# Performance work log

Measured on AMD Instinct MI355X. Metric: run time of the kernel, lower is better.

Reference implementation:

```python
import jax, jax.numpy as jnp
import numpy as np
import math

DIM = 256; SEQ = 2048; BSZ = 32; NI = 128; NS = 4; ITERS = 3

def _ln(x, g, b):
    m = x.mean(-1, keepdims=True)
    v = ((x - m) ** 2).mean(-1, keepdims=True)
    return (x - m) / jnp.sqrt(v + 1e-5) * g + b

def _norm(x):
    # torch F.normalize: x / ||x||.clamp_min(1e-12)
    return x / jnp.clip(jnp.linalg.norm(x, axis=-1, keepdims=True), 1e-12, None)

def setup_inputs() -> dict:
    key = jax.random.key(0)
    ks = jax.random.split(key, 16)
    def w(k, shape, s=0.02):
        return jax.random.normal(k, shape, jnp.float32) * s
    return {
        'tokens': jax.random.normal(ks[0], (BSZ, SEQ, DIM), jnp.float32),
        'cls_embed': jax.random.normal(ks[1], (BSZ, DIM), jnp.float32),
        'intent_queries': jax.random.normal(ks[2], (NI, DIM), jnp.float32),
        'noise': jax.random.normal(ks[3], (NI, BSZ, NS, DIM), jnp.float32),
        'Wk': w(ks[4], (DIM, DIM)), 'bk': jnp.zeros(DIM, jnp.float32),
        'Wv': w(ks[5], (DIM, DIM)), 'bv': jnp.zeros(DIM, jnp.float32),
        'Wqs': w(ks[6], (DIM, DIM)), 'bqs': jnp.zeros(DIM, jnp.float32),
        'Wqi': w(ks[7], (DIM, DIM)), 'bqi': jnp.zeros(DIM, jnp.float32),
        'ln1_g': jnp.ones(DIM, jnp.float32), 'ln1_b': jnp.zeros(DIM, jnp.float32),
        'ln2_g': jnp.ones(DIM, jnp.float32), 'ln2_b': jnp.zeros(DIM, jnp.float32),
        'Wf1': w(ks[8], (DIM, 2 * DIM)), 'bf1': jnp.zeros(2 * DIM, jnp.float32),
        'Wf2': w(ks[9], (2 * DIM, DIM)), 'bf2': jnp.zeros(DIM, jnp.float32),
        'slot_mu': w(ks[10], (1, NS, DIM)),  # randn*0.02
        'slot_sigma': jnp.ones((1, NS, DIM), jnp.float32) * 0.1,
        'alpha': jnp.float32(1.0),
        'temperature': jnp.float32(1.0),
    }

def reference(tokens, cls_embed, intent_queries, noise, Wk, bk, Wv, bv,
              Wqs, bqs, Wqi, bqi, ln1_g, ln1_b, ln2_g, ln2_b,
              Wf1, bf1, Wf2, bf2, slot_mu, slot_sigma, alpha, temperature):
    scale = 1.0 / math.sqrt(DIM)
    # k/v are identical across the per-intent loop in the original -> compute once
    k = tokens @ Wk + bk  # [B,S,D]
    v = tokens @ Wv + bv  # [B,S,D]
    cls_n = _norm(cls_embed)  # [B,D]

    def per_intent(q, eps):  # q: [D], eps: [B,NS,D]
        qn = _norm(q)
        q_intent = (q @ Wqi + bqi)[None, None, :]  # broadcast over [B,NS,:]
        slots = slot_mu[0] + eps * slot_sigma[0]   # [B,NS,D]
        for _ in range(ITERS):
            q_slot = slots @ Wqs + bqs + q_intent
            logit = jnp.einsum('bnd,bsd->bns', q_slot, k) * scale
            attn = jax.nn.softmax(logit, axis=-1)
            upd = jnp.einsum('bns,bsd->bnd', attn, v)
            slots = _ln(slots + upd, ln1_g, ln1_b)
            h = _ln(slots, ln2_g, ln2_b)
            slots = slots + jax.nn.gelu(h @ Wf1 + bf1, approximate=False) @ Wf2 + bf2
        sn = _norm(slots)                               # [B,NS,D]
        a = jax.nn.softmax(jnp.einsum('bnd,d->bn', sn, qn), axis=-1)
        summ = jnp.einsum('bn,bnd->bd', a, slots)       # slot_summary
        fused = cls_n + alpha * _norm(summ)
        return fused @ qn                               # [B]

    scores = jax.vmap(per_intent)(intent_queries, noise)  # [NI,B]
    logits = scores.T / jnp.maximum(temperature, 1e-4)    # [B,NI]
    return logits
```

## Files before the change

### kernel.cpp

```cpp
#include <hip/hip_runtime.h>
#include <math.h>

#define BSZ 32
#define NI  128

typedef __attribute__((ext_vector_type(8))) _Float16 f16x8;
typedef __attribute__((ext_vector_type(4))) _Float16 f16x4;
typedef __attribute__((ext_vector_type(4))) float    f32x4;

#define MFMA16(a, b, c) __builtin_amdgcn_mfma_f32_16x16x32_f16((a), (b), (c), 0, 0, 0)

#define GLL(g, l) __builtin_amdgcn_global_load_lds(                          \
    (const __attribute__((address_space(1))) void*)(g),                      \
    (__attribute__((address_space(3))) void*)(l), 16, 0, 0)

#define LGKM_BAR() do {                                                      \
    asm volatile("s_waitcnt lgkmcnt(0)" ::: "memory");                       \
    __builtin_amdgcn_sched_barrier(0);                                       \
    __builtin_amdgcn_s_barrier();                                            \
    __builtin_amdgcn_sched_barrier(0); } while (0)

__device__ inline float dot4f(float4 a, float4 b) {
    return a.x * b.x + a.y * b.y + a.z * b.z + a.w * b.w;
}

__device__ inline float4* slp(float* base, int r, int c) {
    return (float4*)(base + r * 256 + ((((c) >> 2) ^ (r & 7)) << 2));
}

__device__ inline void tpose64(const float* __restrict__ src, int Csrc,
                               _Float16* __restrict__ dstT, int KT,
                               int r0, int c0, _Float16 (*tbuf)[72], int tid)
{
#pragma unroll
    for (int it = 0; it < 4; it++) {
        int idx = tid + it * 256;
        int rr = idx >> 4, c4 = idx & 15;
        float4 w = *(const float4*)(src + (size_t)(r0 + rr) * Csrc + c0 + c4 * 4);
        tbuf[c4 * 4 + 0][rr] = (_Float16)w.x;
        tbuf[c4 * 4 + 1][rr] = (_Float16)w.y;
        tbuf[c4 * 4 + 2][rr] = (_Float16)w.z;
        tbuf[c4 * 4 + 3][rr] = (_Float16)w.w;
    }
    __syncthreads();
#pragma unroll
    for (int it = 0; it < 2; it++) {
        int idx = tid + it * 256;
        int orr = idx >> 3, oc8 = idx & 7;
        int n = c0 + orr;
        size_t tile = (size_t)(n >> 4) * KT + (r0 >> 5) + (oc8 >> 2);
        *(f16x8*)(dstT + tile * 512 + (n & 15) * 32 + (oc8 & 3) * 8) = *(const f16x8*)&tbuf[orr][oc8 * 8];
    }
}

__global__ __launch_bounds__(256) void prep(
    const float* __restrict__ Wk, const float* __restrict__ Wv,
    const float* __restrict__ Wqs, const float* __restrict__ Wf1,
    const float* __restrict__ Wf2,
    const float* __restrict__ intent_q, const float* __restrict__ Wqi,
    const float* __restrict__ bqi, const float* __restrict__ bqs,
    const float* __restrict__ cls_embed,
    _Float16* __restrict__ wkT, _Float16* __restrict__ wvT,
    _Float16* __restrict__ wqsT, _Float16* __restrict__ wf1T,
    _Float16* __restrict__ wf2T,
    float* __restrict__ qint2, float* __restrict__ qn, float* __restrict__ clsn)
{
    __shared__ _Float16 tbuf[64][72];
    __shared__ float buf[256];
    __shared__ float red[4];
    const int t = threadIdx.x, blk = blockIdx.x;
    const int lane = t & 63, w = t >> 6;

    if (blk < 112) {
        if (blk < 16)       tpose64(Wk, 256, wkT, 8, (blk >> 2) * 64, (blk & 3) * 64, tbuf, t);
        else if (blk < 32)  { int tt = blk - 16; tpose64(Wv, 256, wvT, 8, (tt >> 2) * 64, (tt & 3) * 64, tbuf, t); }
        else if (blk < 48)  { int tt = blk - 32; tpose64(Wqs, 256, wqsT, 8, (tt >> 2) * 64, (tt & 3) * 64, tbuf, t); }
        else if (blk < 80)  { int tt = blk - 48; tpose64(Wf1, 512, wf1T, 8, (tt & 3) * 64, (tt >> 2) * 64, tbuf, t); }
        else                { int tt = blk - 80; tpose64(Wf2, 256, wf2T, 16, (tt >> 2) * 64, (tt & 3) * 64, tbuf, t); }
    } else if (blk < 240) {
        int i = blk - 112;
        float x = intent_q[(size_t)i * 256 + t];
        buf[t] = x;
        float ss = x * x;
#pragma unroll
        for (int m = 1; m < 64; m <<= 1) ss += __shfl_xor(ss, m, 64);
        if (lane == 0) red[w] = ss;
        __syncthreads();
        float tot = red[0] + red[1] + red[2] + red[3];
        qn[(size_t)i * 256 + t] = x / fmaxf(sqrtf(tot), 1e-12f);
        float acc = bqi[t] + bqs[t];
        for (int e = 0; e < 256; e += 4) {
            const float4 q4 = *(const float4*)&buf[e];
            acc += q4.x * Wqi[(size_t)(e + 0) * 256 + t];
            acc += q4.y * Wqi[(size_t)(e + 1) * 256 + t];
            acc += q4.z * Wqi[(size_t)(e + 2) * 256 + t];
            acc += q4.w * Wqi[(size_t)(e + 3) * 256 + t];
        }
        qint2[(size_t)i * 256 + t] = acc;
    } else {
        int b = blk - 240;
        float x = cls_embed[(size_t)b * 256 + t];
        float ss = x * x;
#pragma unroll
        for (int m = 1; m < 64; m <<= 1) ss += __shfl_xor(ss, m, 64);
        if (lane == 0) red[w] = ss;
        __syncthreads();
        float tot = red[0] + red[1] + red[2] + red[3];
        clsn[(size_t)b * 256 + t] = x / fmaxf(sqrtf(tot), 1e-12f);
    }
}

__global__ __launch_bounds__(512, 2) void kvf_k(
    const float* __restrict__ tokens,
    const _Float16* __restrict__ wkT, const _Float16* __restrict__ wvT,
    const float* __restrict__ bk, const float* __restrict__ bv,
    _Float16* __restrict__ kT, _Float16* __restrict__ vT)
{
    __shared__ __align__(16) _Float16 Sb[2][8192];

    const int t = threadIdx.x, lane = t & 63, w = t >> 6;
    const int l15 = lane & 15, quad = lane >> 4;
    const int lofs = l15 * 32 + quad * 8;
    const int lofsA = ((l15 * 4 + quad) ^ ((l15 >> 1) & 7)) * 8;
    const int bx = blockIdx.x;
    const int b = bx & 31, chunk = bx >> 5;

    f16x8 wk[2][8], wv[2][8];
#pragma unroll
    for (int j = 0; j < 2; j++)
#pragma unroll
        for (int ks = 0; ks < 8; ks++) {
            wk[j][ks] = *(const f16x8*)(wkT + ((size_t)(2 * w + j) * 8 + ks) * 512 + lofs);
            wv[j][ks] = *(const f16x8*)(wvT + ((size_t)(2 * w + j) * 8 + ks) * 512 + lofs);
        }
    f32x4 bi0 = *(const f32x4*)(bk + w * 32 + quad * 4);
    f32x4 bi1 = *(const f32x4*)(bk + w * 32 + 16 + quad * 4);
    const float bv0 = bv[(2 * w) * 16 + l15];
    const float bv1 = bv[(2 * w + 1) * 16 + l15];

    const int rr = t >> 5, d8 = t & 31;
    const float* tbase = tokens + ((size_t)b * 2048 + chunk * 256) * 256 + rr * 256 + d8 * 8;
    const int mskW = ((rr >> 1) & 7) ^ (((d8 >> 2) & 3) << 1);
    const int wofs0 = (d8 >> 2) * 512 + (((rr * 4 + (d8 & 3)) ^ mskW) * 8);
    const int wofs1 = wofs0 + 8 * 512;

    float4 pa0, pa1, pb0, pb1;

#define KVF_LOADS(P) do {                                                    \
        const float* sp_ = tbase + (size_t)(P) * 8192;                       \
        pa0 = *(const float4*)(sp_);                                         \
        pa1 = *(const float4*)(sp_ + 4);                                     \
        pb0 = *(const float4*)(sp_ + 4096);                                  \
        pb1 = *(const float4*)(sp_ + 4100);                                  \
    } while (0)

#define KVF_STAGE(BUF) do {                                                  \
        f16x8 h0, h1;                                                        \
        h0[0] = (_Float16)pa0.x; h0[1] = (_Float16)pa0.y;                    \
        h0[2] = (_Float16)pa0.z; h0[3] = (_Float16)pa0.w;                    \
        h0[4] = (_Float16)pa1.x; h0[5] = (_Float16)pa1.y;                    \
        h0[6] = (_Float16)pa1.z; h0[7] = (_Float16)pa1.w;                    \
        h1[0] = (_Float16)pb0.x; h1[1] = (_Float16)pb0.y;                    \
        h1[2] = (_Float16)pb0.z; h1[3] = (_Float16)pb0.w;                    \
        h1[4] = (_Float16)pb1.x; h1[5] = (_Float16)pb1.y;                    \
        h1[6] = (_Float16)pb1.z; h1[7] = (_Float16)pb1.w;                    \
        *(f16x8*)((BUF) + wofs0) = h0;                                       \
        *(f16x8*)((BUF) + wofs1) = h1;                                       \
    } while (0)

    KVF_LOADS(0);
    KVF_STAGE(&Sb[0][0]);
    LGKM_BAR();

    for (int p = 0; p < 8; p++) {
        if (p < 7) KVF_LOADS(p + 1);
        __builtin_amdgcn_sched_barrier(0);

        const _Float16* lb = &Sb[p & 1][0];
        const int stg0 = chunk * 16 + p * 2;
        const int sp = chunk * 8 + p;

        f16x8 a[2][8];
#pragma unroll
        for (int st = 0; st < 2; st++)
#pragma unroll
            for (int ks = 0; ks < 8; ks++)
                a[st][ks] = *(const f16x8*)(lb + (st * 8 + ks) * 512 + (lofsA ^ ((ks & 3) * 16)));

#pragma unroll
        for (int st = 0; st < 2; st++) {
            f32x4 c0 = {0.f, 0.f, 0.f, 0.f}, c1 = {0.f, 0.f, 0.f, 0.f};
#pragma unroll
            for (int ks = 0; ks < 8; ks++) {
                c0 = MFMA16(wk[0][ks], a[st][ks], c0);
                c1 = MFMA16(wk[1][ks], a[st][ks], c1);
            }
            f16x4 p0, p1;
#pragma unroll
            for (int reg = 0; reg < 4; reg++) {
                p0[reg] = (_Float16)(c0[reg] + bi0[reg]);
                p1[reg] = (_Float16)(c1[reg] + bi1[reg]);
            }
            _Float16* tp = kT + ((size_t)(b * 128 + stg0 + st) * 8 + w) * 512 + l15 * 32;
            *(f16x4*)(tp + (quad >> 1) * 8 + (quad & 1) * 4) = p0;
            *(f16x4*)(tp + (2 + (quad >> 1)) * 8 + (quad & 1) * 4) = p1;
        }

#pragma unroll
        for (int j = 0; j < 2; j++) {
            f32x4 c0 = {0.f, 0.f, 0.f, 0.f}, c1 = {0.f, 0.f, 0.f, 0.f};
#pragma unroll
            for (int ks = 0; ks < 8; ks++) {
                c0 = MFMA16(a[0][ks], wv[j][ks], c0);
                c1 = MFMA16(a[1][ks], wv[j][ks], c1);
            }
            const float bb = j ? bv1 : bv0;
            f16x4 p0, p1;
#pragma unroll
            for (int reg = 0; reg < 4; reg++) {
                p0[reg] = (_Float16)(c0[reg] + bb);
                p1[reg] = (_Float16)(c1[reg] + bb);
            }
            _Float16* tp = vT + ((size_t)(b * 16 + 2 * w + j) * 64 + sp) * 512 + l15 * 32;
            *(f16x4*)(tp + (quad >> 1) * 8 + (quad & 1) * 4) = p0;
            *(f16x4*)(tp + (2 + (quad >> 1)) * 8 + (quad & 1) * 4) = p1;
        }

        if (p < 7) {
            KVF_STAGE(&Sb[(p + 1) & 1][0]);
            LGKM_BAR();
        }
    }
#undef KVF_LOADS
#undef KVF_STAGE
}

__global__ __launch_bounds__(256, 4) void slotq_k(
    const float* __restrict__ noise, const float* __restrict__ slot_mu,
    const float* __restrict__ slot_sigma,
    const _Float16* __restrict__ wqsT, const float* __restrict__ qint2,
    float* __restrict__ slots, _Float16* __restrict__ qsT)
{
    __shared__ float sb[16 * 256];
    const int tid = threadIdx.x, lane = tid & 63, w4 = tid >> 6;
    const int l15 = lane & 15, quad = lane >> 4;
    const int lofs = l15 * 32 + quad * 8;
    const int rt = blockIdx.x;
    const int gr0 = rt * 16;

    {
        const int lr = w4 * 4 + quad;
        const int gr = gr0 + lr;
        const int b = gr >> 9, i = (gr >> 2) & 127, n = gr & 3;
        const float* np = noise + (((size_t)i * BSZ + b) * 4 + n) * 256;
#pragma unroll
        for (int k = 0; k < 4; k++) {
            const int c = k * 64 + l15 * 4;
            float4 mu = *(const float4*)(slot_mu + n * 256 + c);
            float4 sg = *(const float4*)(slot_sigma + n * 256 + c);
            float4 ns = *(const float4*)(np + c);
            float4 o;
            o.x = mu.x + ns.x * sg.x; o.y = mu.y + ns.y * sg.y;
            o.z = mu.z + ns.z * sg.z; o.w = mu.w + ns.w * sg.w;
            *slp(sb, lr, c) = o;
            *(float4*)(slots + (size_t)gr * 256 + c) = o;
        }
    }
    __syncthreads();

    f16x8 bs[8];
#pragma unroll
    for (int ks = 0; ks < 8; ks++) {
        const int c0 = ks * 32 + quad * 8;
        float4 xa = *slp(sb, l15, c0);
        float4 xb = *slp(sb, l15, c0 + 4);
        bs[ks][0] = (_Float16)xa.x; bs[ks][1] = (_Float16)xa.y;
        bs[ks][2] = (_Float16)xa.z; bs[ks][3] = (_Float16)xa.w;
        bs[ks][4] = (_Float16)xb.x; bs[ks][5] = (_Float16)xb.y;
        bs[ks][6] = (_Float16)xb.z; bs[ks][7] = (_Float16)xb.w;
    }
    const int iq = ((gr0 + l15) & 511) >> 2;
#pragma unroll
    for (int d = 0; d < 4; d++) {
        const int dti = w4 * 4 + d;
        f32x4 c = {0.f, 0.f, 0.f, 0.f};
#pragma unroll
        for (int ks = 0; ks < 8; ks++)
            c = MFMA16(*(const f16x8*)(wqsT + ((size_t)dti * 8 + ks) * 512 + lofs), bs[ks], c);
        float4 qi = *(const float4*)(qint2 + (size_t)iq * 256 + dti * 16 + quad * 4);
        f16x4 o;
#pragma unroll
        for (int reg = 0; reg < 4; reg++) o[reg] = (_Float16)((c[reg] + qi[reg]) * 0.0625f);
        *(f16x4*)(qsT + ((size_t)rt * 8 + (dti >> 1)) * 512 + l15 * 32
                  + ((dti & 1) * 2 + (quad >> 1)) * 8 + (quad & 1) * 4) = o;
    }
}

__global__ __launch_bounds__(512, 2) void attn_k(
    const _Float16* __restrict__ qsT, const _Float16* __restrict__ kT,
    const _Float16* __restrict__ vT,
    _Float16* __restrict__ Opart, float* __restrict__ psum4)
{
    __shared__ __align__(16) _Float16 Kb[2][16384];
    __shared__ __align__(16) _Float16 Vb[16384];
    __shared__ __align__(16) _Float16 pb[8][2304];

    const int tid = threadIdx.x, lane = tid & 63, wv = tid >> 6;
    const int l15 = lane & 15, quad = lane >> 4;
    const int lofs = l15 * 32 + quad * 8;
    const int lofsA = ((l15 * 4 + quad) ^ ((l15 >> 1) & 7)) * 8;
    const int lnsw = (lane ^ ((lane >> 3) & 7)) * 8;
    const int bx = blockIdx.x;
    const int b = bx & 31, rb = (bx >> 5) & 1, sk = bx >> 6;
    const int gr0 = b * 512 + rb * 256 + wv * 32;
    const int rt_q = gr0 >> 4;

    _Float16* pw = pb[wv];

    const _Float16* kSrc = kT + ((size_t)(b * 128 + sk * 32) * 8) * 512;

    {
        const _Float16* src = kSrc + (size_t)(wv * 4) * 512 + lnsw;
        _Float16* dst = &Kb[0][(wv * 4) * 512 + lane * 8];
#pragma unroll
        for (int j = 0; j < 4; j++) GLL(src + j * 512, dst + j * 512);
    }

    f16x8 q[2][8];
#pragma unroll
    for (int m = 0; m < 2; m++)
#pragma unroll
        for (int ks = 0; ks < 8; ks++)
            q[m][ks] = *(const f16x8*)(qsT + ((size_t)(rt_q + m) * 8 + ks) * 512 + lofs);

    f32x4 O[2][16];
#pragma unroll
    for (int m = 0; m < 2; m++)
#pragma unroll
        for (int dt = 0; dt < 16; dt++) O[m][dt] = (f32x4){0.f, 0.f, 0.f, 0.f};
    float ps[2][4] = {{0.f, 0.f, 0.f, 0.f}, {0.f, 0.f, 0.f, 0.f}};

    asm volatile("s_waitcnt vmcnt(0)" ::: "memory");
    __builtin_amdgcn_s_barrier();
    __builtin_amdgcn_sched_barrier(0);

    for (int s = 0; s < 8; s++) {
        const int cur = s & 1;

        {
            const int seg0 = wv * 4;
#pragma unroll
            for (int j = 0; j < 4; j++) {
                const int seg = seg0 + j;
                const _Float16* src = vT
                    + ((size_t)(b * 16 + (seg >> 1)) * 64 + sk * 16 + s * 2 + (seg & 1)) * 512
                    + lnsw;
                GLL(src, &Vb[seg * 512 + lane * 8]);
            }
        }
        if (s < 7) {
            const _Float16* src = kSrc + (size_t)(s + 1) * 16384 + (wv * 4) * 512 + lnsw;
            _Float16* dst = &Kb[cur ^ 1][(wv * 4) * 512 + lane * 8];
#pragma unroll
            for (int j = 0; j < 4; j++) GLL(src + j * 512, dst + j * 512);
            asm volatile("s_waitcnt vmcnt(8)" ::: "memory");
        } else {
            asm volatile("s_waitcnt vmcnt(4)" ::: "memory");
        }
        __builtin_amdgcn_s_barrier();
        __builtin_amdgcn_sched_barrier(0);

#pragma unroll
        for (int kt = 0; kt < 4; kt++) {
            const _Float16* kp = &Kb[cur][(kt * 8) * 512];
            f32x4 c0 = {0.f, 0.f, 0.f, 0.f}, c1 = {0.f, 0.f, 0.f, 0.f};
#pragma unroll
            for (int ks = 0; ks < 8; ks++) {
                f16x8 kf = *(const f16x8*)(kp + ks * 512 + lofsA);
                c0 = MFMA16(q[0][ks], kf, c0);
                c1 = MFMA16(q[1][ks], kf, c1);
            }
            const int col = kt * 16 + l15;
#pragma unroll
            for (int reg = 0; reg < 4; reg++) {
                float p0 = __expf(fminf(c0[reg], 10.5f));
                float p1 = __expf(fminf(c1[reg], 10.5f));
                ps[0][reg] += p0;
                ps[1][reg] += p1;
                pw[(quad * 4 + reg) * 72 + col] = (_Float16)p0;
                pw[(16 + quad * 4 + reg) * 72 + col] = (_Float16)p1;
            }
        }

        __builtin_amdgcn_sched_barrier(0);
        if (s < 7) {
            asm volatile("s_waitcnt vmcnt(4)" ::: "memory");
        } else {
            asm volatile("s_waitcnt vmcnt(0)" ::: "memory");
        }
        __builtin_amdgcn_s_barrier();
        __builtin_amdgcn_sched_barrier(0);

        f16x8 pa[2][2];
#pragma unroll
        for (int m = 0; m < 2; m++)
#pragma unroll
            for (int kg = 0; kg < 2; kg++)
                pa[m][kg] = *(const f16x8*)(pw + (m * 16 + l15) * 72 + kg * 32 + quad * 8);
#pragma unroll
        for (int dt = 0; dt < 16; dt++) {
            const _Float16* vp = &Vb[dt * 1024];
            f16x8 v0 = *(const f16x8*)(vp + lofsA);
            f16x8 v1 = *(const f16x8*)(vp + 512 + lofsA);
            O[0][dt] = MFMA16(pa[0][0], v0, O[0][dt]);
            O[0][dt] = MFMA16(pa[0][1], v1, O[0][dt]);
            O[1][dt] = MFMA16(pa[1][0], v0, O[1][dt]);
            O[1][dt] = MFMA16(pa[1][1], v1, O[1][dt]);
        }

        __builtin_amdgcn_sched_barrier(0);
        __builtin_amdgcn_s_barrier();
        __builtin_amdgcn_sched_barrier(0);
    }

#pragma unroll
    for (int m = 0; m < 2; m++) {
#pragma unroll
        for (int msk = 1; msk <= 8; msk <<= 1)
#pragma unroll
            for (int reg = 0; reg < 4; reg++) ps[m][reg] += __shfl_xor(ps[m][reg], msk, 64);
        if (l15 == 0) {
#pragma unroll
            for (int reg = 0; reg < 4; reg++)
                psum4[(size_t)sk * 16384 + gr0 + m * 16 + quad * 4 + reg] = ps[m][reg];
        }
    }

#pragma unroll
    for (int m = 0; m < 2; m++) {
#pragma unroll
        for (int hd = 0; hd < 2; hd++) {
#pragma unroll
            for (int dt = 0; dt < 8; dt++) {
                const int dti = hd * 8 + dt;
#pragma unroll
                for (int reg = 0; reg < 4; reg++)
                    pw[(quad * 4 + reg) * 136 + dt * 16 + l15] = (_Float16)O[m][dti][reg];
            }
#pragma unroll
            for (int p2 = 0; p2 < 4; p2++) {
                const int u = lane + p2 * 64;
                const int row = u >> 4, col8 = u & 15;
                *(f16x8*)(Opart + ((size_t)sk * 16384 + gr0 + m * 16 + row) * 256 + hd * 128 + col8 * 8) =
                    *(const f16x8*)(pw + row * 136 + col8 * 8);
            }
        }
    }
}

__global__ __launch_bounds__(256, 4) void mlp_k(
    const _Float16* __restrict__ Opart, const float* __restrict__ psum4,
    float* __restrict__ slots,
    const float* __restrict__ ln1_g, const float* __restrict__ ln1_b,
    const float* __restrict__ ln2_g, const float* __restrict__ ln2_b,
    const _Float16* __restrict__ wf1T, const float* __restrict__ bf1,
    const _Float16* __restrict__ wf2T, const float* __restrict__ bf2,
    const _Float16* __restrict__ wqsT, const float* __restrict__ qint2,
    _Float16* __restrict__ qsT,
    const float* __restrict__ qn, const float* __restrict__ clsn,
    const float* __restrict__ alphap, const float* __restrict__ tempp,
    float* __restrict__ out, int it)
{
    __shared__ float sl[16 * 256];
    __shared__ float2 st2[16];
    __shared__ __align__(16) _Float16 actL[8192];

    const int tid = threadIdx.x, lane = tid & 63, w4 = tid >> 6;
    const int l15 = lane & 15, quad = lane >> 4;
    const int lofs = l15 * 32 + quad * 8;
    const int lofsA = ((l15 * 4 + quad) ^ ((l15 >> 1) & 7)) * 8;
    const int bx = blockIdx.x;
    const int b = bx & 31, rg = bx >> 5;
    const int R0 = b * 512 + rg * 16;

    {
        const int lr = w4 * 4 + quad;
        const int gr = R0 + lr;
        float l = 0.f;
#pragma unroll
        for (int j = 0; j < 4; j++) l += psum4[(size_t)j * 16384 + gr];
        const float invl = 1.f / l;
        float4 y[4];
        float sm = 0.f, sq = 0.f;
#pragma unroll
        for (int k = 0; k < 4; k++) {
            const int c = k * 64 + l15 * 4;
            float4 o4 = {0.f, 0.f, 0.f, 0.f};
#pragma unroll
            for (int j = 0; j < 4; j++) {
                f16x4 p = *(const f16x4*)(Opart + ((size_t)j * 16384 + gr) * 256 + c);
                o4.x += (float)p[0]; o4.y += (float)p[1];
                o4.z += (float)p[2]; o4.w += (float)p[3];
            }
            float4 s4 = *(const float4*)(slots + (size_t)gr * 256 + c);
            y[k].x = s4.x + o4.x * invl; y[k].y = s4.y + o4.y * invl;
            y[k].z = s4.z + o4.z * invl; y[k].w = s4.w + o4.w * invl;
            sm += y[k].x + y[k].y + y[k].z + y[k].w;
            sq += dot4f(y[k], y[k]);
        }
#pragma unroll
        for (int m = 1; m <= 8; m <<= 1) { sm += __shfl_xor(sm, m, 64); sq += __shfl_xor(sq, m, 64); }
        const float mean = sm * (1.f / 256.f);
        const float rstd = rsqrtf(sq * (1.f / 256.f) - mean * mean + 1e-5f);
        float sm2 = 0.f, sq2 = 0.f;
#pragma unroll
        for (int k = 0; k < 4; k++) {
            const int c = k * 64 + l15 * 4;
            float4 g1 = *(const float4*)(ln1_g + c);
            float4 b1 = *(const float4*)(ln1_b + c);
            float4 x1;
            x1.x = (y[k].x - mean) * rstd * g1.x + b1.x;
            x1.y = (y[k].y - mean) * rstd * g1.y + b1.y;
            x1.z = (y[k].z - mean) * rstd * g1.z + b1.z;
            x1.w = (y[k].w - mean) * rstd * g1.w + b1.w;
            *slp(sl, lr, c) = x1;
            sm2 += x1.x + x1.y + x1.z + x1.w;
            sq2 += dot4f(x1, x1);
        }
#pragma unroll
        for (int m = 1; m <= 8; m <<= 1) { sm2 += __shfl_xor(sm2, m, 64); sq2 += __shfl_xor(sq2, m, 64); }
        const float mean2 = sm2 * (1.f / 256.f);
        const float rstd2 = rsqrtf(sq2 * (1.f / 256.f) - mean2 * mean2 + 1e-5f);
        if (l15 == 0) st2[lr] = make_float2(mean2, rstd2);
    }
    __syncthreads();

    {
        const float2 s2 = st2[l15];
        f16x8 bh[8];
#pragma unroll
        for (int ks = 0; ks < 8; ks++) {
            const int c0 = ks * 32 + quad * 8;
            float4 xa = *slp(sl, l15, c0);
            float4 xb = *slp(sl, l15, c0 + 4);
            float4 ga = *(const float4*)(ln2_g + c0);
            float4 gb = *(const float4*)(ln2_g + c0 + 4);
            float4 ba = *(const float4*)(ln2_b + c0);
            float4 bb2 = *(const float4*)(ln2_b + c0 + 4);
            bh[ks][0] = (_Float16)((xa.x - s2.x) * s2.y * ga.x + ba.x);
            bh[ks][1] = (_Float16)((xa.y - s2.x) * s2.y * ga.y + ba.y);
            bh[ks][2] = (_Float16)((xa.z - s2.x) * s2.y * ga.z + ba.z);
            bh[ks][3] = (_Float16)((xa.w - s2.x) * s2.y * ga.w + ba.w);
            bh[ks][4] = (_Float16)((xb.x - s2.x) * s2.y * gb.x + bb2.x);
            bh[ks][5] = (_Float16)((xb.y - s2.x) * s2.y * gb.y + bb2.y);
            bh[ks][6] = (_Float16)((xb.z - s2.x) * s2.y * gb.z + bb2.z);
            bh[ks][7] = (_Float16)((xb.w - s2.x) * s2.y * gb.w + bb2.w);
        }
#pragma unroll 2
        for (int t8 = 0; t8 < 8; t8++) {
            const int hti = w4 * 8 + t8;
            f32x4 c = {0.f, 0.f, 0.f, 0.f};
#pragma unroll
            for (int ks = 0; ks < 8; ks++)
                c = MFMA16(*(const f16x8*)(wf1T + ((size_t)hti * 8 + ks) * 512 + lofs), bh[ks], c);
            float4 bb = *(const float4*)(bf1 + hti * 16 + quad * 4);
            f16x4 o;
#pragma unroll
            for (int reg = 0; reg < 4; reg++) {
                float xg = c[reg] + bb[reg];
                o[reg] = (_Float16)(0.5f * xg * (1.f + erff(xg * 0.70710678118654752f)));
            }
            const int gA = l15 * 4 + (hti & 1) * 2 + (quad >> 1);
            *(f16x4*)(actL + ((size_t)(hti >> 1)) * 512
                      + ((gA ^ ((l15 >> 1) & 7)) * 8) + (quad & 1) * 4) = o;
        }
    }
    __syncthreads();

    {
        f32x4 c[4];
#pragma unroll
        for (int d = 0; d < 4; d++) {
            const int dti = w4 * 4 + d;
            float4 x4 = *slp(sl, l15, dti * 16 + quad * 4);
            float4 bb = *(const float4*)(bf2 + dti * 16 + quad * 4);
            c[d] = (f32x4){x4.x + bb.x, x4.y + bb.y, x4.z + bb.z, x4.w + bb.w};
        }
        for (int ks = 0; ks < 16; ks++) {
            f16x8 afrag = *(const f16x8*)(actL + (size_t)ks * 512 + lofsA);
#pragma unroll
            for (int d = 0; d < 4; d++)
                c[d] = MFMA16(*(const f16x8*)(wf2T + ((size_t)(w4 * 4 + d) * 16 + ks) * 512 + lofs),
                              afrag, c[d]);
        }
        __syncthreads();
#pragma unroll
        for (int d = 0; d < 4; d++) {
            const int dti = w4 * 4 + d;
            float4 v = {c[d][0], c[d][1], c[d][2], c[d][3]};
            *slp(sl, l15, dti * 16 + quad * 4) = v;
        }
    }
    __syncthreads();

    if (it < 2) {
        f16x8 bs[8];
#pragma unroll
        for (int ks = 0; ks < 8; ks++) {
            const int c0 = ks * 32 + quad * 8;
            float4 xa = *slp(sl, l15, c0);
            float4 xb = *slp(sl, l15, c0 + 4);
            bs[ks][0] = (_Float16)xa.x; bs[ks][1] = (_Float16)xa.y;
            bs[ks][2] = (_Float16)xa.z; bs[ks][3] = (_Float16)xa.w;
            bs[ks][4] = (_Float16)xb.x; bs[ks][5] = (_Float16)xb.y;
            bs[ks][6] = (_Float16)xb.z; bs[ks][7] = (_Float16)xb.w;
        }
        const int iq = rg * 4 + (l15 >> 2);
        const int rtg = b * 32 + rg;
#pragma unroll
        for (int d = 0; d < 4; d++) {
            const int dti = w4 * 4 + d;
            f32x4 c = {0.f, 0.f, 0.f, 0.f};
#pragma unroll
            for (int ks = 0; ks < 8; ks++)
                c = MFMA16(*(const f16x8*)(wqsT + ((size_t)dti * 8 + ks) * 512 + lofs), bs[ks], c);
            float4 qi = *(const float4*)(qint2 + (size_t)iq * 256 + dti * 16 + quad * 4);
            f16x4 o;
#pragma unroll
            for (int reg = 0; reg < 4; reg++) o[reg] = (_Float16)((c[reg] + qi[reg]) * 0.0625f);
            *(f16x4*)(qsT + ((size_t)rtg * 8 + (dti >> 1)) * 512 + l15 * 32
                      + ((dti & 1) * 2 + (quad >> 1)) * 8 + (quad & 1) * 4) = o;
        }
        {
            const int lr2 = tid >> 4, c16 = tid & 15;
#pragma unroll
            for (int q4 = 0; q4 < 4; q4++) {
                float4 v = *slp(sl, lr2, c16 * 16 + q4 * 4);
                *(float4*)(slots + (size_t)(R0 + lr2) * 256 + c16 * 16 + q4 * 4) = v;
            }
        }
    } else {
        const int i = rg * 4 + w4;
        float4 qv = *(const float4*)(qn + (size_t)i * 256 + lane * 4);
        float4 xs[4];
        float st4[4];
#pragma unroll
        for (int n = 0; n < 4; n++) {
            xs[n] = *slp(sl, w4 * 4 + n, lane * 4);
            float ss = dot4f(xs[n], xs[n]);
            float sq = dot4f(xs[n], qv);
#pragma unroll
            for (int m = 1; m < 64; m <<= 1) { ss += __shfl_xor(ss, m, 64); sq += __shfl_xor(sq, m, 64); }
            st4[n] = sq / fmaxf(sqrtf(ss), 1e-12f);
        }
        float mx = fmaxf(fmaxf(st4[0], st4[1]), fmaxf(st4[2], st4[3]));
        float e0 = __expf(st4[0] - mx), e1 = __expf(st4[1] - mx);
        float e2 = __expf(st4[2] - mx), e3 = __expf(st4[3] - mx);
        float inv = 1.f / (e0 + e1 + e2 + e3);
        float4 smv;
        smv.x = (e0 * xs[0].x + e1 * xs[1].x + e2 * xs[2].x + e3 * xs[3].x) * inv;
        smv.y = (e0 * xs[0].y + e1 * xs[1].y + e2 * xs[2].y + e3 * xs[3].y) * inv;
        smv.z = (e0 * xs[0].z + e1 * xs[1].z + e2 * xs[2].z + e3 * xs[3].z) * inv;
        smv.w = (e0 * xs[0].w + e1 * xs[1].w + e2 * xs[2].w + e3 * xs[3].w) * inv;
        float ssm = dot4f(smv, smv);
        float sqn = dot4f(smv, qv);
        float4 cv = *(const float4*)(clsn + (size_t)b * 256 + lane * 4);
        float cq = dot4f(cv, qv);
#pragma unroll
        for (int m = 1; m < 64; m <<= 1) {
            ssm += __shfl_xor(ssm, m, 64);
            sqn += __shfl_xor(sqn, m, 64);
            cq  += __shfl_xor(cq,  m, 64);
        }
        if (lane == 0) {
            float score = cq + alphap[0] * sqn / fmaxf(sqrtf(ssm), 1e-12f);
            out[(size_t)b * NI + i] = score / fmaxf(tempp[0], 1e-4f);
        }
    }
}

extern "C" void kernel_launch(void* const* d_in, const int* in_sizes, int n_in,
                              void* d_out, int out_size, void* d_ws, size_t ws_size,
                              hipStream_t stream)
{
    const float* tokens     = (const float*)d_in[0];
    const float* cls_embed  = (const float*)d_in[1];
    const float* intent_q   = (const float*)d_in[2];
    const float* noise      = (const float*)d_in[3];
    const float* Wk  = (const float*)d_in[4];
    const float* bk  = (const float*)d_in[5];
    const float* Wv  = (const float*)d_in[6];
    const float* bv  = (const float*)d_in[7];
    const float* Wqs = (const float*)d_in[8];
    const float* bqs = (const float*)d_in[9];
    const float* Wqi = (const float*)d_in[10];
    const float* bqi = (const float*)d_in[11];
    const float* ln1g = (const float*)d_in[12];
    const float* ln1b = (const float*)d_in[13];
    const float* ln2g = (const float*)d_in[14];
    const float* ln2b = (const float*)d_in[15];
    const float* Wf1 = (const float*)d_in[16];
    const float* bf1 = (const float*)d_in[17];
    const float* Wf2 = (const float*)d_in[18];
    const float* bf2 = (const float*)d_in[19];
    const float* slot_mu    = (const float*)d_in[20];
    const float* slot_sigma = (const float*)d_in[21];
    const float* alphap = (const float*)d_in[22];
    const float* tempp  = (const float*)d_in[23];
    float* out = (float*)d_out;

    char* base = (char*)d_ws;
    _Float16* qsT   = (_Float16*)(base);
    _Float16* kT    = (_Float16*)(base + 33554432u);
    _Float16* vT    = (_Float16*)(base + 67108864u);
    _Float16* Opart = (_Float16*)(base + 100663296u);
    float* slots    = (float*)(base + 134217728u);
    _Float16* wkT   = (_Float16*)(base + 150994944u);
    _Float16* wvT   = (_Float16*)(base + 151126016u);
    _Float16* wqsT  = (_Float16*)(base + 151257088u);
    _Float16* wf1T  = (_Float16*)(base + 151388160u);
    _Float16* wf2T  = (_Float16*)(base + 151650304u);
    float* qint2    = (float*)(base + 151912448u);
    float* qnb      = (float*)(base + 152043520u);
    float* clsn     = (float*)(base + 152174592u);
    float* psum4    = (float*)(base + 152207360u);

    prep<<<272, 256, 0, stream>>>(Wk, Wv, Wqs, Wf1, Wf2, intent_q, Wqi, bqi, bqs,
                                  cls_embed, wkT, wvT, wqsT, wf1T, wf2T,
                                  qint2, qnb, clsn);
    kvf_k<<<256, 512, 0, stream>>>(tokens, wkT, wvT, bk, bv, kT, vT);
    slotq_k<<<1024, 256, 0, stream>>>(noise, slot_mu, slot_sigma, wqsT, qint2,
                                      slots, qsT);

    for (int it = 0; it < 3; it++) {
        attn_k<<<256, 512, 0, stream>>>(qsT, kT, vT, Opart, psum4);
        mlp_k<<<1024, 256, 0, stream>>>(Opart, psum4, slots,
                                        ln1g, ln1b, ln2g, ln2b,
                                        wf1T, bf1, wf2T, bf2,
                                        wqsT, qint2, qsT,
                                        qnb, clsn, alphap, tempp, out, it);
    }
}
```

Measured before the change: 473.6 us.

## Halve rows per wave in attention kernel to double grid and occupancy

The attention kernel now gives each wave 16 query rows instead of 32 and processes the key range in 16 smaller steps of 32 keys. It launches 512 blocks instead of 256 with launch bounds of 4 blocks per CU. Shared memory shrinks because the K, V and P buffers are smaller and the output staging reuses the K/V arena. The aim is higher occupancy and better latency hiding, at the cost of half the K/V reuse per block, twice as many global loads of K/V, and more barriers per key.

```diff
diff --git a/kernel.cpp b/kernel.cpp
--- a/kernel.cpp
+++ b/kernel.cpp
@@ -296,14 +296,16 @@
     }
 }
 
-__global__ __launch_bounds__(512, 2) void attn_k(
+__global__ __launch_bounds__(512, 4) void attn_k(
     const _Float16* __restrict__ qsT, const _Float16* __restrict__ kT,
     const _Float16* __restrict__ vT,
     _Float16* __restrict__ Opart, float* __restrict__ psum4)
 {
-    __shared__ __align__(16) _Float16 Kb[2][16384];
-    __shared__ __align__(16) _Float16 Vb[16384];
-    __shared__ __align__(16) _Float16 pb[8][2304];
+    __shared__ __align__(16) _Float16 arena[24576];
+    __shared__ __align__(16) _Float16 pb[8][640];
+
+    _Float16* KbA = arena;
+    _Float16* VbA = arena + 16384;
 
     const int tid = threadIdx.x, lane = tid & 63, wv = tid >> 6;
     const int l15 = lane & 15, quad = lane >> 4;
@@ -311,149 +313,121 @@
     const int lofsA = ((l15 * 4 + quad) ^ ((l15 >> 1) & 7)) * 8;
     const int lnsw = (lane ^ ((lane >> 3) & 7)) * 8;
     const int bx = blockIdx.x;
-    const int b = bx & 31, rb = (bx >> 5) & 1, sk = bx >> 6;
-    const int gr0 = b * 512 + rb * 256 + wv * 32;
+    const int b = bx & 31, rb = (bx >> 5) & 3, sk = bx >> 7;
+    const int gr0 = b * 512 + rb * 128 + wv * 16;
     const int rt_q = gr0 >> 4;
 
     _Float16* pw = pb[wv];
 
     const _Float16* kSrc = kT + ((size_t)(b * 128 + sk * 32) * 8) * 512;
-
-    {
-        const _Float16* src = kSrc + (size_t)(wv * 4) * 512 + lnsw;
-        _Float16* dst = &Kb[0][(wv * 4) * 512 + lane * 8];
-#pragma unroll
-        for (int j = 0; j < 4; j++) GLL(src + j * 512, dst + j * 512);
-    }
-
-    f16x8 q[2][8];
-#pragma unroll
-    for (int m = 0; m < 2; m++)
-#pragma unroll
-        for (int ks = 0; ks < 8; ks++)
-            q[m][ks] = *(const f16x8*)(qsT + ((size_t)(rt_q + m) * 8 + ks) * 512 + lofs);
-
-    f32x4 O[2][16];
-#pragma unroll
-    for (int m = 0; m < 2; m++)
-#pragma unroll
-        for (int dt = 0; dt < 16; dt++) O[m][dt] = (f32x4){0.f, 0.f, 0.f, 0.f};
-    float ps[2][4] = {{0.f, 0.f, 0.f, 0.f}, {0.f, 0.f, 0.f, 0.f}};
+    const _Float16* vSrc = vT + ((size_t)(b * 16) * 64 + sk * 16) * 512;
+
+#pragma unroll
+    for (int j = 0; j < 2; j++) {
+        const int ee = wv * 2 + j;
+        GLL(kSrc + (size_t)((ee >> 3) * 8 + (ee & 7)) * 512 + lnsw,
+            KbA + ee * 512 + lane * 8);
+    }
+
+    f16x8 q[8];
+#pragma unroll
+    for (int ks = 0; ks < 8; ks++)
+        q[ks] = *(const f16x8*)(qsT + ((size_t)rt_q * 8 + ks) * 512 + lofs);
+
+    f32x4 O[16];
+#pragma unroll
+    for (int dt = 0; dt < 16; dt++) O[dt] = (f32x4){0.f, 0.f, 0.f, 0.f};
+    float ps[4] = {0.f, 0.f, 0.f, 0.f};
 
     asm volatile("s_waitcnt vmcnt(0)" ::: "memory");
     __builtin_amdgcn_s_barrier();
     __builtin_amdgcn_sched_barrier(0);
 
-    for (int s = 0; s < 8; s++) {
-        const int cur = s & 1;
-
-        {
-            const int seg0 = wv * 4;
-#pragma unroll
-            for (int j = 0; j < 4; j++) {
-                const int seg = seg0 + j;
-                const _Float16* src = vT
-                    + ((size_t)(b * 16 + (seg >> 1)) * 64 + sk * 16 + s * 2 + (seg & 1)) * 512
-                    + lnsw;
-                GLL(src, &Vb[seg * 512 + lane * 8]);
-            }
-        }
-        if (s < 7) {
-            const _Float16* src = kSrc + (size_t)(s + 1) * 16384 + (wv * 4) * 512 + lnsw;
-            _Float16* dst = &Kb[cur ^ 1][(wv * 4) * 512 + lane * 8];
-#pragma unroll
-            for (int j = 0; j < 4; j++) GLL(src + j * 512, dst + j * 512);
-            asm volatile("s_waitcnt vmcnt(8)" ::: "memory");
+    for (int ss = 0; ss < 16; ss++) {
+        const int cur = ss & 1;
+
+#pragma unroll
+        for (int j = 0; j < 2; j++) {
+            const int ee = wv * 2 + j;
+            GLL(vSrc + (size_t)(ee * 64 + ss) * 512 + lnsw, VbA + ee * 512 + lane * 8);
+        }
+        if (ss < 15) {
+#pragma unroll
+            for (int j = 0; j < 2; j++) {
+                const int ee = wv * 2 + j;
+                GLL(kSrc + (size_t)((2 * (ss + 1) + (ee >> 3)) * 8 + (ee & 7)) * 512 + lnsw,
+                    KbA + (cur ^ 1) * 8192 + ee * 512 + lane * 8);
+            }
+            asm volatile("s_waitcnt vmcnt(4)" ::: "memory");
         } else {
-            asm volatile("s_waitcnt vmcnt(4)" ::: "memory");
+            asm volatile("s_waitcnt vmcnt(2)" ::: "memory");
         }
         __builtin_amdgcn_s_barrier();
         __builtin_amdgcn_sched_barrier(0);
 
 #pragma unroll
-        for (int kt = 0; kt < 4; kt++) {
-            const _Float16* kp = &Kb[cur][(kt * 8) * 512];
-            f32x4 c0 = {0.f, 0.f, 0.f, 0.f}, c1 = {0.f, 0.f, 0.f, 0.f};
-#pragma unroll
-            for (int ks = 0; ks < 8; ks++) {
-                f16x8 kf = *(const f16x8*)(kp + ks * 512 + lofsA);
-                c0 = MFMA16(q[0][ks], kf, c0);
-                c1 = MFMA16(q[1][ks], kf, c1);
-            }
+        for (int kt = 0; kt < 2; kt++) {
+            const _Float16* kp = KbA + cur * 8192 + (kt * 8) * 512;
+            f32x4 c0 = {0.f, 0.f, 0.f, 0.f};
+#pragma unroll
+            for (int ks = 0; ks < 8; ks++)
+                c0 = MFMA16(q[ks], *(const f16x8*)(kp + ks * 512 + lofsA), c0);
             const int col = kt * 16 + l15;
 #pragma unroll
             for (int reg = 0; reg < 4; reg++) {
                 float p0 = __expf(fminf(c0[reg], 10.5f));
-                float p1 = __expf(fminf(c1[reg], 10.5f));
-                ps[0][reg] += p0;
-                ps[1][reg] += p1;
-                pw[(quad * 4 + reg) * 72 + col] = (_Float16)p0;
-                pw[(16 + quad * 4 + reg) * 72 + col] = (_Float16)p1;
+                ps[reg] += p0;
+                pw[(quad * 4 + reg) * 40 + col] = (_Float16)p0;
             }
         }
 
         __builtin_amdgcn_sched_barrier(0);
-        if (s < 7) {
-            asm volatile("s_waitcnt vmcnt(4)" ::: "memory");
+        asm volatile("s_waitcnt lgkmcnt(0)" ::: "memory");
+        if (ss < 15) {
+            asm volatile("s_waitcnt vmcnt(2)" ::: "memory");
         } else {
             asm volatile("s_waitcnt vmcnt(0)" ::: "memory");
         }
         __builtin_amdgcn_s_barrier();
         __builtin_amdgcn_sched_barrier(0);
 
-        f16x8 pa[2][2];
-#pragma unroll
-        for (int m = 0; m < 2; m++)
-#pragma unroll
-            for (int kg = 0; kg < 2; kg++)
-                pa[m][kg] = *(const f16x8*)(pw + (m * 16 + l15) * 72 + kg * 32 + quad * 8);
-#pragma unroll
-        for (int dt = 0; dt < 16; dt++) {
-            const _Float16* vp = &Vb[dt * 1024];
-            f16x8 v0 = *(const f16x8*)(vp + lofsA);
-            f16x8 v1 = *(const f16x8*)(vp + 512 + lofsA);
-            O[0][dt] = MFMA16(pa[0][0], v0, O[0][dt]);
-            O[0][dt] = MFMA16(pa[0][1], v1, O[0][dt]);
-            O[1][dt] = MFMA16(pa[1][0], v0, O[1][dt]);
-            O[1][dt] = MFMA16(pa[1][1], v1, O[1][dt]);
-        }
-
+        {
+            f16x8 pa = *(const f16x8*)(pw + l15 * 40 + quad * 8);
+#pragma unroll
+            for (int dt = 0; dt < 16; dt++)
+                O[dt] = MFMA16(pa, *(const f16x8*)(VbA + dt * 512 + lofsA), O[dt]);
+        }
         __builtin_amdgcn_sched_barrier(0);
         __builtin_amdgcn_s_barrier();
         __builtin_amdgcn_sched_barrier(0);
     }
 
 #pragma unroll
-    for (int m = 0; m < 2; m++) {
-#pragma unroll
-        for (int msk = 1; msk <= 8; msk <<= 1)
-#pragma unroll
-            for (int reg = 0; reg < 4; reg++) ps[m][reg] += __shfl_xor(ps[m][reg], msk, 64);
-        if (l15 == 0) {
+    for (int msk = 1; msk <= 8; msk <<= 1)
+#pragma unroll
+        for (int reg = 0; reg < 4; reg++) ps[reg] += __shfl_xor(ps[reg], msk, 64);
+    if (l15 == 0) {
+#pragma unroll
+        for (int reg = 0; reg < 4; reg++)
+            psum4[(size_t)sk * 16384 + gr0 + quad * 4 + reg] = ps[reg];
+    }
+
+    _Float16* ow = arena + wv * 2176;
+#pragma unroll
+    for (int hd = 0; hd < 2; hd++) {
+#pragma unroll
+        for (int dt = 0; dt < 8; dt++) {
+            const int dti = hd * 8 + dt;
 #pragma unroll
             for (int reg = 0; reg < 4; reg++)
-                psum4[(size_t)sk * 16384 + gr0 + m * 16 + quad * 4 + reg] = ps[m][reg];
-        }
-    }
-
-#pragma unroll
-    for (int m = 0; m < 2; m++) {
-#pragma unroll
-        for (int hd = 0; hd < 2; hd++) {
-#pragma unroll
-            for (int dt = 0; dt < 8; dt++) {
-                const int dti = hd * 8 + dt;
-#pragma unroll
-                for (int reg = 0; reg < 4; reg++)
-                    pw[(quad * 4 + reg) * 136 + dt * 16 + l15] = (_Float16)O[m][dti][reg];
-            }
-#pragma unroll
-            for (int p2 = 0; p2 < 4; p2++) {
-                const int u = lane + p2 * 64;
-                const int row = u >> 4, col8 = u & 15;
-                *(f16x8*)(Opart + ((size_t)sk * 16384 + gr0 + m * 16 + row) * 256 + hd * 128 + col8 * 8) =
-                    *(const f16x8*)(pw + row * 136 + col8 * 8);
-            }
+                ow[(quad * 4 + reg) * 136 + dt * 16 + l15] = (_Float16)O[dti][reg];
+        }
+#pragma unroll
+        for (int p2 = 0; p2 < 4; p2++) {
+            const int u = lane + p2 * 64;
+            const int row = u >> 4, col8 = u & 15;
+            *(f16x8*)(Opart + ((size_t)sk * 16384 + gr0 + row) * 256 + hd * 128 + col8 * 8) =
+                *(const f16x8*)(ow + row * 136 + col8 * 8);
         }
     }
 }
@@ -733,7 +707,7 @@
                                       slots, qsT);
 
     for (int it = 0; it < 3; it++) {
-        attn_k<<<256, 512, 0, stream>>>(qsT, kT, vT, Opart, psum4);
+        attn_k<<<512, 512, 0, stream>>>(qsT, kT, vT, Opart, psum4);
         mlp_k<<<1024, 256, 0, stream>>>(Opart, psum4, slots,
                                         ln1g, ln1b, ln2g, ln2b,
                                         wf1T, bf1, wf2T, bf2,
```

Result: slower. 489.3 us (+3.3%).
